# Kernel optimization log

Measured on AMD Instinct MI355X. Metric: run time of the kernel, lower is better.

## Reference

```python
import jax, jax.numpy as jnp
import numpy as np

DIM = 192; HEADS = 6; HD = DIM // HEADS
WS = 8; SS = 4; N = WS * WS
B = 4; H = 256; W = 256
SCALE = HD ** -0.5

def _rpi(ws):
    coords = np.stack(np.meshgrid(np.arange(ws), np.arange(ws), indexing='ij'))  # (2, ws, ws)
    cf = coords.reshape(2, -1)
    rel = (cf[:, :, None] - cf[:, None, :]).transpose(1, 2, 0)  # (N, N, 2)
    rel[:, :, 0] += ws - 1
    rel[:, :, 1] += ws - 1
    rel[:, :, 0] *= 2 * ws - 1
    return rel.sum(-1).reshape(-1)  # (N*N,)

def _attn_mask(h, w, ws, ss):
    if ss == 0:
        return None
    img = np.zeros((h, w))
    cnt = 0
    for hs in (slice(0, -ws), slice(-ws, -ss), slice(-ss, None)):
        for wsl in (slice(0, -ws), slice(-ws, -ss), slice(-ss, None)):
            img[hs, wsl] = cnt; cnt += 1
    mw = img.reshape(h // ws, ws, w // ws, ws).transpose(0, 2, 1, 3).reshape(-1, ws * ws)
    am = mw[:, None, :] - mw[:, :, None]
    return jnp.asarray(np.where(am != 0, -100.0, 0.0), dtype=jnp.float32)  # (nW, N, N)

RPI = jnp.asarray(_rpi(WS))            # (N*N,) int
MASK = _attn_mask(H, W, WS, SS)        # (nW, N, N) or None
NW = (H // WS) * (W // WS)

def setup_inputs() -> dict:
    key = jax.random.key(0)
    ks = jax.random.split(key, 4)
    return {
        'x': jax.random.normal(ks[0], (B, DIM, H, W), dtype=jnp.float32),
        'qkv_w': jax.random.normal(ks[1], (3 * DIM, DIM), dtype=jnp.float32) * 0.02,
        'qkv_b': jnp.zeros((3 * DIM,), dtype=jnp.float32),
        'proj_w': jax.random.normal(ks[2], (DIM, DIM), dtype=jnp.float32) * 0.02,
        'proj_b': jnp.zeros((DIM,), dtype=jnp.float32),
        'rpb_table': jax.random.normal(ks[3], ((2 * WS - 1) ** 2, HEADS), dtype=jnp.float32) * 0.02,
    }

def reference(x, qkv_w, qkv_b, proj_w, proj_b, rpb_table):
    # cyclic shift
    xs = jnp.roll(x, shift=(-SS, -SS), axis=(2, 3))
    # NCHW -> NHWC, partition into (B*nW, N, C) windows
    xh = xs.transpose(0, 2, 3, 1)
    xw = xh.reshape(B, H // WS, WS, W // WS, WS, DIM).transpose(0, 1, 3, 2, 4, 5).reshape(-1, N, DIM)
    # qkv projection
    qkv = (xw @ qkv_w.T + qkv_b).reshape(-1, N, 3, HEADS, HD).transpose(2, 0, 3, 1, 4)
    q, k, v = qkv[0], qkv[1], qkv[2]  # (B_, heads, N, HD)
    attn = jnp.einsum('bhqd,bhkd->bhqk', q * SCALE, k)  # (B_, heads, N, N)
    # relative position bias: (N*N, heads) -> (heads, N, N)
    bias = rpb_table[RPI].reshape(N, N, HEADS).transpose(2, 0, 1)
    attn = attn + bias[None]
    if MASK is not None:
        attn = attn.reshape(B, NW, HEADS, N, N) + MASK[None, :, None]
        attn = attn.reshape(-1, HEADS, N, N)
    attn = jax.nn.softmax(attn, axis=-1)
    out = jnp.einsum('bhqk,bhkd->bhqd', attn, v).transpose(0, 2, 1, 3).reshape(-1, N, DIM)
    out = out @ proj_w.T + proj_b
    # reverse window partition -> NHWC -> NCHW, reverse shift
    out = out.reshape(B, H // WS, W // WS, WS, WS, DIM).transpose(0, 1, 3, 2, 4, 5).reshape(B, H, W, DIM)
    out = out.transpose(0, 3, 1, 2)
    return jnp.roll(out, shift=(SS, SS), axis=(2, 3))
```

## Files before the change

### kernel.cpp

```cpp
#include <hip/hip_runtime.h>

namespace {

typedef float floatx4 __attribute__((ext_vector_type(4)));
typedef short bf16x8  __attribute__((ext_vector_type(8)));

constexpr int   kThreads = 384;
constexpr float kScale   = 0.17677669529663687f;

__device__ inline short f2bf(float f){
    unsigned u = __builtin_bit_cast(unsigned, f);
    unsigned r = (u + 0x7fffu + ((u >> 16) & 1u)) >> 16;
    return (short)r;
}

__device__ inline floatx4 mfma16(bf16x8 a, bf16x8 b, floatx4 c){
    return __builtin_amdgcn_mfma_f32_16x16x32_bf16(a, b, c, 0, 0, 0);
}

__device__ inline bf16x8 ldwfrag(const float* wrow, const short* prow,
                                 int use_pk, int cs, int grp){
    if (use_pk){
        return *(const bf16x8*)(prow + cs * 32 + grp * 8);
    }
    const float* p = wrow + cs * 32 + grp * 4;
    float4 a = *(const float4*)p;
    float4 b = *(const float4*)(p + 16);
    bf16x8 r;
    r[0] = f2bf(a.x); r[1] = f2bf(a.y); r[2] = f2bf(a.z); r[3] = f2bf(a.w);
    r[4] = f2bf(b.x); r[5] = f2bf(b.y); r[6] = f2bf(b.z); r[7] = f2bf(b.w);
    return r;
}

__global__ void pack_w(const float* __restrict__ qkv_w,
                       const float* __restrict__ proj_w,
                       short* __restrict__ wpk){
    int idx = blockIdx.x * 256 + threadIdx.x;
    if (idx >= 768 * 192) return;
    int row = idx / 192, c = idx % 192;
    float v = (row < 576) ? qkv_w[row * 192 + c] : proj_w[(row - 576) * 192 + c];
    int cs = c >> 5, c5 = c & 31;
    int grp = (c5 & 15) >> 2;
    int j = (c5 & 3) | ((c5 >> 4) << 2);
    wpk[row * 192 + cs * 32 + grp * 8 + j] = f2bf(v);
}

__global__ __launch_bounds__(kThreads)
void swin_mfma(const float* __restrict__ x, const float* __restrict__ qkv_w,
               const float* __restrict__ qkv_b, const float* __restrict__ proj_w,
               const float* __restrict__ proj_b, const float* __restrict__ rpb,
               float* __restrict__ out, const short* __restrict__ wpk, int use_pk)
{
    __shared__ __align__(16) short xf[6][4][64][8];
    __shared__ __align__(16) short of[6][4][64][8];
    __shared__ float rpb_s[1350];
    __shared__ float qb_s[576];
    __shared__ float pb_s[192];
    __shared__ int   rgn_s[64];

    const int t      = threadIdx.x;
    const int lane   = t & 63;
    const int wv     = t >> 6;
    const int tok_lo = lane & 15;
    const int grp    = lane >> 4;

    const int win = blockIdx.x;
    const int b = win >> 10, wh = (win >> 5) & 31, ww = win & 31;

    for (int i = t; i < 1350; i += kThreads) rpb_s[i] = rpb[i];
    for (int i = t; i < 576;  i += kThreads) qb_s[i]  = qkv_b[i];
    if (t < 192) pb_s[t] = proj_b[t];
    if (t < 64){
        int r = t >> 3, c = t & 7;
        int hs = wh * 8 + r, wsx = ww * 8 + c;
        int rg = (hs < 248) ? 0 : ((hs < 252) ? 1 : 2);
        int cg = (wsx < 248) ? 0 : ((wsx < 252) ? 1 : 2);
        rgn_s[t] = rg * 3 + cg;
    }
    {
        const size_t xbase = (size_t)b * 192 * 65536;
        #pragma unroll
        for (int c0 = 0; c0 < 4; ++c0){
            int comb = c0 * 6 + wv;
            int cs = comb >> 2, tt = comb & 3;
            int tok = tok_lo + 16 * tt;
            int rr = tok >> 3, cc = tok & 7;
            int h = (wh * 8 + rr + 4) & 255;
            int w = (ww * 8 + cc + 4) & 255;
            const float* xp = x + xbase + h * 256 + w;
            bf16x8 f;
            #pragma unroll
            for (int j = 0; j < 8; ++j){
                int ch = 32 * cs + 4 * grp + (j & 3) + 16 * (j >> 2);
                f[j] = f2bf(xp[(size_t)ch << 16]);
            }
            *(bf16x8*)&xf[cs][tt][lane][0] = f;
        }
    }
    __syncthreads();

    const int hd = wv;

    floatx4 qa[2][4], ka[2][4], va[4][2];
    {
        floatx4 z = {0.f, 0.f, 0.f, 0.f};
        #pragma unroll
        for (int o = 0; o < 2; ++o)
            #pragma unroll
            for (int tt = 0; tt < 4; ++tt){ qa[o][tt] = z; ka[o][tt] = z; va[tt][o] = z; }
    }
    const int rq0 = 32 * hd + tok_lo;
    #pragma unroll
    for (int cs = 0; cs < 6; ++cs){
        bf16x8 wq[2], wk[2], wvv[2];
        #pragma unroll
        for (int o = 0; o < 2; ++o){
            int r1 = rq0 + 16 * o;
            wq[o]  = ldwfrag(qkv_w + (size_t)r1 * 192,         wpk + (size_t)r1 * 192,         use_pk, cs, grp);
            wk[o]  = ldwfrag(qkv_w + (size_t)(192 + r1) * 192, wpk + (size_t)(192 + r1) * 192, use_pk, cs, grp);
            wvv[o] = ldwfrag(qkv_w + (size_t)(384 + r1) * 192, wpk + (size_t)(384 + r1) * 192, use_pk, cs, grp);
        }
        #pragma unroll
        for (int tt = 0; tt < 4; ++tt){
            bf16x8 xb = *(const bf16x8*)&xf[cs][tt][lane][0];
            qa[0][tt] = mfma16(wq[0], xb, qa[0][tt]);
            qa[1][tt] = mfma16(wq[1], xb, qa[1][tt]);
            ka[0][tt] = mfma16(wk[0], xb, ka[0][tt]);
            ka[1][tt] = mfma16(wk[1], xb, ka[1][tt]);
            va[tt][0] = mfma16(xb, wvv[0], va[tt][0]);
            va[tt][1] = mfma16(xb, wvv[1], va[tt][1]);
        }
    }

    bf16x8 Qf[4], Kf[4], Vf[2][2];
    {
        float qb[8], kb[8];
        #pragma unroll
        for (int j = 0; j < 8; ++j){
            int d = 16 * (j >> 2) + 4 * grp + (j & 3);
            qb[j] = qb_s[32 * hd + d];
            kb[j] = qb_s[192 + 32 * hd + d];
        }
        #pragma unroll
        for (int tt = 0; tt < 4; ++tt){
            bf16x8 fq, fk;
            #pragma unroll
            for (int j = 0; j < 8; ++j){
                int o = j >> 2, r = j & 3;
                fq[j] = f2bf((qa[o][tt][r] + qb[j]) * kScale);
                fk[j] = f2bf( ka[o][tt][r] + kb[j]);
            }
            Qf[tt] = fq; Kf[tt] = fk;
        }
        #pragma unroll
        for (int it = 0; it < 2; ++it){
            float vb = qb_s[384 + 32 * hd + 16 * it + tok_lo];
            #pragma unroll
            for (int ks = 0; ks < 2; ++ks){
                bf16x8 f;
                #pragma unroll
                for (int j = 0; j < 8; ++j){
                    int r = j & 3, tt = 2 * ks + (j >> 2);
                    f[j] = f2bf(va[tt][it][r] + vb);
                }
                Vf[it][ks] = f;
            }
        }
    }

    float s[4][4][4];
    {
        floatx4 z = {0.f, 0.f, 0.f, 0.f};
        #pragma unroll
        for (int kt = 0; kt < 4; ++kt)
            #pragma unroll
            for (int qt = 0; qt < 4; ++qt){
                floatx4 sv = mfma16(Kf[kt], Qf[qt], z);
                #pragma unroll
                for (int r = 0; r < 4; ++r) s[kt][qt][r] = sv[r];
            }
    }
    {
        const int qrb = tok_lo >> 3, qc = tok_lo & 7;
        const int krb = grp >> 1,    kc0 = 4 * (grp & 1);
        int rq[4];
        #pragma unroll
        for (int qt = 0; qt < 4; ++qt) rq[qt] = rgn_s[16 * qt + tok_lo];
        #pragma unroll
        for (int kt = 0; kt < 4; ++kt){
            int rk[4];
            #pragma unroll
            for (int r = 0; r < 4; ++r) rk[r] = rgn_s[16 * kt + 4 * grp + r];
            #pragma unroll
            for (int qt = 0; qt < 4; ++qt){
                int base = (2 * qt + qrb - 2 * kt - krb + 7) * 15 + (qc - kc0 + 7);
                #pragma unroll
                for (int r = 0; r < 4; ++r){
                    float add = rpb_s[(base - r) * 6 + hd];
                    if (rk[r] != rq[qt]) add -= 100.f;
                    s[kt][qt][r] += add;
                }
            }
        }
    }
    float inv[4];
    #pragma unroll
    for (int qt = 0; qt < 4; ++qt){
        float m = -1e30f;
        #pragma unroll
        for (int kt = 0; kt < 4; ++kt)
            #pragma unroll
            for (int r = 0; r < 4; ++r) m = fmaxf(m, s[kt][qt][r]);
        m = fmaxf(m, __shfl_xor(m, 16));
        m = fmaxf(m, __shfl_xor(m, 32));
        float sum = 0.f;
        #pragma unroll
        for (int kt = 0; kt < 4; ++kt)
            #pragma unroll
            for (int r = 0; r < 4; ++r){
                float e = __expf(s[kt][qt][r] - m);
                s[kt][qt][r] = e; sum += e;
            }
        sum += __shfl_xor(sum, 16);
        sum += __shfl_xor(sum, 32);
        inv[qt] = 1.0f / sum;
    }

    floatx4 oa[2][4];
    {
        floatx4 z = {0.f, 0.f, 0.f, 0.f};
        #pragma unroll
        for (int it = 0; it < 2; ++it)
            #pragma unroll
            for (int qt = 0; qt < 4; ++qt) oa[it][qt] = z;
    }
    #pragma unroll
    for (int ks = 0; ks < 2; ++ks)
        #pragma unroll
        for (int qt = 0; qt < 4; ++qt){
            bf16x8 pf;
            #pragma unroll
            for (int j = 0; j < 8; ++j) pf[j] = f2bf(s[2 * ks + (j >> 2)][qt][j & 3]);
            oa[0][qt] = mfma16(Vf[0][ks], pf, oa[0][qt]);
            oa[1][qt] = mfma16(Vf[1][ks], pf, oa[1][qt]);
        }
    #pragma unroll
    for (int qt = 0; qt < 4; ++qt){
        bf16x8 f;
        #pragma unroll
        for (int j = 0; j < 8; ++j){
            int it = j >> 2, r = j & 3;
            f[j] = f2bf(oa[it][qt][r] * inv[qt]);
        }
        *(bf16x8*)&of[wv][qt][lane][0] = f;
    }
    __syncthreads();

    floatx4 pa[2][4];
    {
        floatx4 z = {0.f, 0.f, 0.f, 0.f};
        #pragma unroll
        for (int o = 0; o < 2; ++o)
            #pragma unroll
            for (int tt = 0; tt < 4; ++tt) pa[o][tt] = z;
    }
    #pragma unroll
    for (int h2 = 0; h2 < 6; ++h2){
        bf16x8 pw[2];
        #pragma unroll
        for (int o = 0; o < 2; ++o){
            int och = 32 * wv + 16 * o + tok_lo;
            pw[o] = ldwfrag(proj_w + (size_t)och * 192,
                            wpk + (size_t)(576 + och) * 192, use_pk, h2, grp);
        }
        #pragma unroll
        for (int tt = 0; tt < 4; ++tt){
            bf16x8 ob = *(const bf16x8*)&of[h2][tt][lane][0];
            pa[0][tt] = mfma16(pw[0], ob, pa[0][tt]);
            pa[1][tt] = mfma16(pw[1], ob, pa[1][tt]);
        }
    }

    #pragma unroll
    for (int o = 0; o < 2; ++o)
        #pragma unroll
        for (int tt = 0; tt < 4; ++tt){
            int tok = tok_lo + 16 * tt;
            int rr = tok >> 3, cc = tok & 7;
            int h = (wh * 8 + rr + 4) & 255;
            int w = (ww * 8 + cc + 4) & 255;
            #pragma unroll
            for (int r = 0; r < 4; ++r){
                int och = 32 * wv + 16 * o + 4 * grp + r;
                out[((size_t)(b * 192 + och) << 16) + (h << 8) + w]
                    = pa[o][tt][r] + pb_s[och];
            }
        }
}

}

extern "C" void kernel_launch(void* const* d_in, const int* in_sizes, int n_in,
                              void* d_out, int out_size, void* d_ws, size_t ws_size,
                              hipStream_t stream) {
    (void)in_sizes; (void)n_in; (void)out_size;
    const float* x      = (const float*)d_in[0];
    const float* qkv_w  = (const float*)d_in[1];
    const float* qkv_b  = (const float*)d_in[2];
    const float* proj_w = (const float*)d_in[3];
    const float* proj_b = (const float*)d_in[4];
    const float* rpb    = (const float*)d_in[5];
    float* out = (float*)d_out;
    short* wpk = (short*)d_ws;

    const int use_pk = (ws_size >= (size_t)(768 * 192 * 2)) ? 1 : 0;
    if (use_pk) pack_w<<<576, 256, 0, stream>>>(qkv_w, proj_w, wpk);
    swin_mfma<<<4096, kThreads, 0, stream>>>(x, qkv_w, qkv_b, proj_w, proj_b,
                                             rpb, out, wpk, use_pk);
}
```

Measured before the change: 747.7 us.

## Alias LDS fragment buffers, raise occupancy, swizzle block order, drop weight prepack

The x and output fragment buffers now share one LDS array, with an extra barrier before the overwrite, and launch bounds request 5 blocks per CU for higher occupancy. Block indices are remapped so consecutive blocks land on different batch/window regions, spreading the strided x reads differently across caches. The separate bf16 weight pre-pack kernel is removed, so weights are now converted from fp32 inside the kernel. That saves a launch but adds conversion work and doubles weight read bytes. The register cap from the launch bound may cause spills.

```diff
diff --git a/kernel.cpp b/kernel.cpp
--- a/kernel.cpp
+++ b/kernel.cpp
@@ -18,11 +18,7 @@
     return __builtin_amdgcn_mfma_f32_16x16x32_bf16(a, b, c, 0, 0, 0);
 }
 
-__device__ inline bf16x8 ldwfrag(const float* wrow, const short* prow,
-                                 int use_pk, int cs, int grp){
-    if (use_pk){
-        return *(const bf16x8*)(prow + cs * 32 + grp * 8);
-    }
+__device__ inline bf16x8 ldwfrag(const float* __restrict__ wrow, int cs, int grp){
     const float* p = wrow + cs * 32 + grp * 4;
     float4 a = *(const float4*)p;
     float4 b = *(const float4*)(p + 16);
@@ -32,27 +28,13 @@
     return r;
 }
 
-__global__ void pack_w(const float* __restrict__ qkv_w,
-                       const float* __restrict__ proj_w,
-                       short* __restrict__ wpk){
-    int idx = blockIdx.x * 256 + threadIdx.x;
-    if (idx >= 768 * 192) return;
-    int row = idx / 192, c = idx % 192;
-    float v = (row < 576) ? qkv_w[row * 192 + c] : proj_w[(row - 576) * 192 + c];
-    int cs = c >> 5, c5 = c & 31;
-    int grp = (c5 & 15) >> 2;
-    int j = (c5 & 3) | ((c5 >> 4) << 2);
-    wpk[row * 192 + cs * 32 + grp * 8 + j] = f2bf(v);
-}
-
-__global__ __launch_bounds__(kThreads)
+__global__ __launch_bounds__(kThreads, 5)
 void swin_mfma(const float* __restrict__ x, const float* __restrict__ qkv_w,
                const float* __restrict__ qkv_b, const float* __restrict__ proj_w,
                const float* __restrict__ proj_b, const float* __restrict__ rpb,
-               float* __restrict__ out, const short* __restrict__ wpk, int use_pk)
+               float* __restrict__ out)
 {
-    __shared__ __align__(16) short xf[6][4][64][8];
-    __shared__ __align__(16) short of[6][4][64][8];
+    __shared__ __align__(16) short frag[6][4][64][8];
     __shared__ float rpb_s[1350];
     __shared__ float qb_s[576];
     __shared__ float pb_s[192];
@@ -64,7 +46,8 @@
     const int tok_lo = lane & 15;
     const int grp    = lane >> 4;
 
-    const int win = blockIdx.x;
+    const int bid = blockIdx.x;
+    const int win = (bid & 7) * 512 + (bid >> 3);
     const int b = win >> 10, wh = (win >> 5) & 31, ww = win & 31;
 
     for (int i = t; i < 1350; i += kThreads) rpb_s[i] = rpb[i];
@@ -94,7 +77,7 @@
                 int ch = 32 * cs + 4 * grp + (j & 3) + 16 * (j >> 2);
                 f[j] = f2bf(xp[(size_t)ch << 16]);
             }
-            *(bf16x8*)&xf[cs][tt][lane][0] = f;
+            *(bf16x8*)&frag[cs][tt][lane][0] = f;
         }
     }
     __syncthreads();
@@ -116,13 +99,13 @@
         #pragma unroll
         for (int o = 0; o < 2; ++o){
             int r1 = rq0 + 16 * o;
-            wq[o]  = ldwfrag(qkv_w + (size_t)r1 * 192,         wpk + (size_t)r1 * 192,         use_pk, cs, grp);
-            wk[o]  = ldwfrag(qkv_w + (size_t)(192 + r1) * 192, wpk + (size_t)(192 + r1) * 192, use_pk, cs, grp);
-            wvv[o] = ldwfrag(qkv_w + (size_t)(384 + r1) * 192, wpk + (size_t)(384 + r1) * 192, use_pk, cs, grp);
+            wq[o]  = ldwfrag(qkv_w + (size_t)r1 * 192,         cs, grp);
+            wk[o]  = ldwfrag(qkv_w + (size_t)(192 + r1) * 192, cs, grp);
+            wvv[o] = ldwfrag(qkv_w + (size_t)(384 + r1) * 192, cs, grp);
         }
         #pragma unroll
         for (int tt = 0; tt < 4; ++tt){
-            bf16x8 xb = *(const bf16x8*)&xf[cs][tt][lane][0];
+            bf16x8 xb = *(const bf16x8*)&frag[cs][tt][lane][0];
             qa[0][tt] = mfma16(wq[0], xb, qa[0][tt]);
             qa[1][tt] = mfma16(wq[1], xb, qa[1][tt]);
             ka[0][tt] = mfma16(wk[0], xb, ka[0][tt]);
@@ -244,6 +227,9 @@
             oa[0][qt] = mfma16(Vf[0][ks], pf, oa[0][qt]);
             oa[1][qt] = mfma16(Vf[1][ks], pf, oa[1][qt]);
         }
+
+    __syncthreads();
+
     #pragma unroll
     for (int qt = 0; qt < 4; ++qt){
         bf16x8 f;
@@ -252,7 +238,7 @@
             int it = j >> 2, r = j & 3;
             f[j] = f2bf(oa[it][qt][r] * inv[qt]);
         }
-        *(bf16x8*)&of[wv][qt][lane][0] = f;
+        *(bf16x8*)&frag[wv][qt][lane][0] = f;
     }
     __syncthreads();
 
@@ -270,12 +256,11 @@
         #pragma unroll
         for (int o = 0; o < 2; ++o){
             int och = 32 * wv + 16 * o + tok_lo;
-            pw[o] = ldwfrag(proj_w + (size_t)och * 192,
-                            wpk + (size_t)(576 + och) * 192, use_pk, h2, grp);
+            pw[o] = ldwfrag(proj_w + (size_t)och * 192, h2, grp);
         }
         #pragma unroll
         for (int tt = 0; tt < 4; ++tt){
-            bf16x8 ob = *(const bf16x8*)&of[h2][tt][lane][0];
+            bf16x8 ob = *(const bf16x8*)&frag[h2][tt][lane][0];
             pa[0][tt] = mfma16(pw[0], ob, pa[0][tt]);
             pa[1][tt] = mfma16(pw[1], ob, pa[1][tt]);
         }
@@ -303,7 +288,7 @@
 extern "C" void kernel_launch(void* const* d_in, const int* in_sizes, int n_in,
                               void* d_out, int out_size, void* d_ws, size_t ws_size,
                               hipStream_t stream) {
-    (void)in_sizes; (void)n_in; (void)out_size;
+    (void)in_sizes; (void)n_in; (void)out_size; (void)d_ws; (void)ws_size;
     const float* x      = (const float*)d_in[0];
     const float* qkv_w  = (const float*)d_in[1];
     const float* qkv_b  = (const float*)d_in[2];
@@ -311,10 +296,7 @@
     const float* proj_b = (const float*)d_in[4];
     const float* rpb    = (const float*)d_in[5];
     float* out = (float*)d_out;
-    short* wpk = (short*)d_ws;
-
-    const int use_pk = (ws_size >= (size_t)(768 * 192 * 2)) ? 1 : 0;
-    if (use_pk) pack_w<<<576, 256, 0, stream>>>(qkv_w, proj_w, wpk);
+
     swin_mfma<<<4096, kThreads, 0, stream>>>(x, qkv_w, qkv_b, proj_w, proj_b,
-                                             rpb, out, wpk, use_pk);
-}
+                                             rpb, out);
+}
```

New measurement: 1.568 ms. 110% more time.
